# Kernel optimization log

Hardware: AMD Instinct MI355X
Metric: run time of the kernel (lower is better)

The kernel has to match this reference:

```python
import jax, jax.numpy as jnp
import numpy as np

QBITS = 8
QMIN, QMAX = -(2 ** (QBITS - 1)), 2 ** (QBITS - 1) - 1  # qint8: -128..127


def fq_act(x):
    """Per-tensor affine fake-quant (observer = min/max of tensor), with STE."""
    mn = jnp.minimum(jnp.min(x), 0.0)
    mx = jnp.maximum(jnp.max(x), 0.0)
    scale = jnp.maximum((mx - mn) / (QMAX - QMIN), 1e-8)
    zp = QMIN - jnp.round(mn / scale)
    q = jnp.clip(jnp.round(x / scale) + zp, QMIN, QMAX)
    y = (q - zp) * scale
    return x + jax.lax.stop_gradient(y - x)


def fq_w(w):
    """Per-tensor symmetric weight fake-quant, with STE."""
    scale = jnp.maximum(jnp.max(jnp.abs(w)) / QMAX, 1e-8)
    y = jnp.clip(jnp.round(w / scale), QMIN, QMAX) * scale
    return w + jax.lax.stop_gradient(y - w)


def setup_inputs() -> dict:
    key = jax.random.key(0)
    ks = jax.random.split(key, 8)
    B, T, F, K = 32, 1024, 512, 31
    return {
        "x": jax.random.normal(ks[0], (B, T, F), jnp.float32),
        "ln_scale": jnp.ones((F,), jnp.float32),
        "ln_bias": jnp.zeros((F,), jnp.float32),
        "w1": jax.random.normal(ks[1], (2 * F, F), jnp.float32) * 0.02,
        "b1": jax.random.normal(ks[2], (2 * F,), jnp.float32) * 0.02,
        "dw_w": jax.random.normal(ks[3], (F, 1, K), jnp.float32) * 0.1,
        "dw_b": jax.random.normal(ks[4], (F,), jnp.float32) * 0.02,
        "bn_gamma": jnp.ones((F,), jnp.float32),
        "bn_beta": jnp.zeros((F,), jnp.float32),
        "bn_mean": jnp.zeros((F,), jnp.float32),
        "bn_var": jax.random.uniform(ks[5], (F,), jnp.float32, 0.5, 1.5),
        "w2": jax.random.normal(ks[6], (F, F), jnp.float32) * 0.02,
        "b2": jax.random.normal(ks[7], (F,), jnp.float32) * 0.02,
    }


def reference(x, ln_scale, ln_bias, w1, b1, dw_w, dw_b,
              bn_gamma, bn_beta, bn_mean, bn_var, w2, b2):
    F = x.shape[-1]
    # --- custom L1 layer norm, fake-quant in/out ---
    t = fq_act(x)
    t = t - jnp.mean(t, axis=-1, keepdims=True)
    t = t / (jnp.sum(jnp.abs(t), axis=-1, keepdims=True) / F + 1e-5)
    t = t * ln_scale + ln_bias
    t = fq_act(t)
    # --- pointwise conv 1 (linear F -> 2F), quant-wrapped ---
    t = fq_act(t)
    t = jnp.einsum("btf,of->bto", t, fq_w(w1)) + b1
    t = fq_act(t)
    # --- GLU, quant-wrapped ---
    t = fq_act(t)
    a, g = jnp.split(t, 2, axis=-1)
    t = a * jax.nn.sigmoid(g)
    t = fq_act(t)
    # --- depthwise conv over time, quant-wrapped ---
    t = jnp.transpose(t, (0, 2, 1))  # [B,F,T]
    t = fq_act(t)
    t = jax.lax.conv_general_dilated(
        t, fq_w(dw_w), window_strides=(1,), padding=[((dw_w.shape[-1] - 1) // 2,) * 2],
        dimension_numbers=("NCH", "OIH", "NCH"), feature_group_count=F,
    ) + dw_b[:, None]
    t = fq_act(t)
    # --- batch norm (eval mode, running stats), quant-wrapped ---
    t = fq_act(t)
    t = (t - bn_mean[:, None]) * (bn_gamma[:, None] / jnp.sqrt(bn_var[:, None] + 1e-5)) + bn_beta[:, None]
    t = fq_act(t)
    t = jnp.transpose(t, (0, 2, 1))  # [B,T,F]
    # --- SiLU activation, quant-wrapped ---
    t = fq_act(t)
    t = jax.nn.silu(t)
    t = fq_act(t)
    # --- pointwise conv 2 (linear F -> F), quant-wrapped ---
    t = fq_act(t)
    t = jnp.einsum("btf,of->bto", t, fq_w(w2)) + b2
    t = fq_act(t)
    return t  # dropout is identity at eval
```

## Files before the change

### kernel.cpp

```cpp
#include <hip/hip_runtime.h>
#include <stdint.h>
#include <math.h>

#define INF __builtin_inff()

typedef __attribute__((ext_vector_type(4))) float f32x4;
typedef __attribute__((ext_vector_type(8))) short s16x8;
typedef __attribute__((ext_vector_type(4))) short s16x4;
typedef __attribute__((ext_vector_type(4))) char c8x4;

#define S_XMN 0
#define S_XMX 1
#define S_T1MN 2
#define S_T1MX 3
#define S_T4MN 4
#define S_T4MX 5
#define S_T7MN 6
#define S_T7MX 7
#define S_CVMN 8
#define S_CVMX 9
#define S_BNMN 10
#define S_BNMX 11
#define S_SIMN 12
#define S_SIMX 13
#define S_T18MN 14
#define S_T18MX 15
#define S_W1 16
#define S_W2 17
#define S_DW 18
#define NSLOT 19

#define NTOT 16777216L

__device__ __forceinline__ unsigned enc(float f) {
  unsigned u = __float_as_uint(f);
  return (u & 0x80000000u) ? ~u : (u | 0x80000000u);
}
__device__ __forceinline__ float dec(unsigned k) {
  return (k & 0x80000000u) ? __uint_as_float(k & 0x7FFFFFFFu) : __uint_as_float(~k);
}

struct FQ { float s, zp; };

__device__ __forceinline__ FQ fq_params(float mn_t, float mx_t) {
  float mn = fminf(mn_t, 0.0f), mx = fmaxf(mx_t, 0.0f);
  FQ p;
  p.s = fmaxf((mx - mn) / 255.0f, 1e-8f);
  p.zp = -128.0f - rintf(mn / p.s);
  return p;
}
__device__ __forceinline__ float fq_apply(float x, FQ p) {
  float q = rintf(x / p.s) + p.zp;
  q = fminf(fmaxf(q, -128.0f), 127.0f);
  return (q - p.zp) * p.s;
}
__device__ __forceinline__ float fq_qmz(float x, FQ p) {
  float q = rintf(x / p.s) + p.zp;
  q = fminf(fmaxf(q, -128.0f), 127.0f);
  return q - p.zp;
}
__device__ __forceinline__ int qidx(float x, FQ p) {
  float q = rintf(x / p.s) + p.zp;
  q = fminf(fmaxf(q, -128.0f), 127.0f);
  return (int)q + 128;
}
__device__ __forceinline__ void fq_pair(const unsigned* slots, int idx, FQ& p1, FQ& p2) {
  float mn = dec(slots[idx]), mx = dec(slots[idx + 1]);
  p1 = fq_params(mn, mx);
  float ymn = fq_apply(mn, p1), ymx = fq_apply(mx, p1);
  p2 = fq_params(ymn, ymx);
}
__device__ __forceinline__ unsigned short to_bf16(float v) {
  return (unsigned short)(__float_as_uint(v) >> 16);
}

__device__ __forceinline__ void mm_block_atomic(float mn, float mx, unsigned* smn, unsigned* smx) {
#pragma unroll
  for (int o = 32; o > 0; o >>= 1) {
    mn = fminf(mn, __shfl_down(mn, o, 64));
    mx = fmaxf(mx, __shfl_down(mx, o, 64));
  }
  __shared__ float rmn[16], rmx[16];
  int lane = threadIdx.x & 63, wid = threadIdx.x >> 6;
  int nw = blockDim.x >> 6;
  __syncthreads();
  if (lane == 0) { rmn[wid] = mn; rmx[wid] = mx; }
  __syncthreads();
  if (threadIdx.x == 0) {
    for (int i = 1; i < nw; ++i) { mn = fminf(mn, rmn[i]); mx = fmaxf(mx, rmx[i]); }
    atomicMin(smn, enc(mn));
    atomicMax(smx, enc(mx));
  }
}

__device__ __forceinline__ float wave_sum(float v) {
#pragma unroll
  for (int o = 1; o < 64; o <<= 1) v += __shfl_xor(v, o, 64);
  return v;
}

__global__ void k_init(unsigned* __restrict__ slots, const float* __restrict__ gm,
                       const float* __restrict__ vr, float* __restrict__ gs) {
  int i = threadIdx.x;
  if (i < NSLOT) slots[i] = (i < 16) ? ((i & 1) ? enc(-INF) : enc(INF)) : enc(0.0f);
  gs[i] = gm[i] / sqrtf(vr[i] + 1e-5f);
}

__global__ __launch_bounds__(256) void k_redmm(const float* __restrict__ x, unsigned* __restrict__ slots) {
  long i = ((long)blockIdx.x * 256 + threadIdx.x) * 4;
  const long stride = (long)2048 * 256 * 4;
  float mn = INF, mx = -INF;
  for (; i < NTOT; i += stride) {
    f32x4 v = *(const f32x4*)(x + i);
    mn = fminf(mn, fminf(fminf(v.x, v.y), fminf(v.z, v.w)));
    mx = fmaxf(mx, fmaxf(fmaxf(v.x, v.y), fmaxf(v.z, v.w)));
  }
  mm_block_atomic(mn, mx, slots + S_XMN, slots + S_XMX);
}

__global__ __launch_bounds__(256) void k_wabs(const float* __restrict__ w1, const float* __restrict__ w2,
                                              const float* __restrict__ dw, unsigned* __restrict__ slots) {
  int b = blockIdx.x;
  const float* p; int slot; long base;
  if (b < 2048) { p = w1; slot = S_W1; base = (long)b * 256; }
  else if (b < 3072) { p = w2; slot = S_W2; base = (long)(b - 2048) * 256; }
  else { p = dw; slot = S_DW; base = (long)(b - 3072) * 256; }
  float v = fabsf(p[base + threadIdx.x]);
#pragma unroll
  for (int o = 32; o > 0; o >>= 1) v = fmaxf(v, __shfl_down(v, o, 64));
  __shared__ float r[4];
  int lane = threadIdx.x & 63, wid = threadIdx.x >> 6;
  if (lane == 0) r[wid] = v;
  __syncthreads();
  if (threadIdx.x == 0) {
    v = fmaxf(fmaxf(r[0], r[1]), fmaxf(r[2], r[3]));
    atomicMax(slots + slot, enc(v));
  }
}

__global__ __launch_bounds__(256) void k_wq(const float* __restrict__ w1, const float* __restrict__ w2,
    const float* __restrict__ dw, unsigned short* __restrict__ w1q, unsigned short* __restrict__ w2q,
    float* __restrict__ dwq, const unsigned* __restrict__ slots) {
  int b = blockIdx.x;
  if (b < 2048) {
    float s = fmaxf(dec(slots[S_W1]) / 127.0f, 1e-8f);
    long i = (long)b * 256 + threadIdx.x;
    float q = fminf(fmaxf(rintf(w1[i] / s), -128.0f), 127.0f);
    w1q[i] = to_bf16(q);
  } else if (b < 3072) {
    float s = fmaxf(dec(slots[S_W2]) / 127.0f, 1e-8f);
    long i = (long)(b - 2048) * 256 + threadIdx.x;
    float q = fminf(fmaxf(rintf(w2[i] / s), -128.0f), 127.0f);
    w2q[i] = to_bf16(q);
  } else {
    float s = fmaxf(dec(slots[S_DW]) / 127.0f, 1e-8f);
    long i = (long)(b - 3072) * 256 + threadIdx.x;
    float q = fminf(fmaxf(rintf(dw[i] / s), -128.0f), 127.0f);
    dwq[i] = q;
  }
}

__device__ __forceinline__ void ln_row_wave(const float* __restrict__ xr, int lane, FQ p0,
    const f32x4& sc0, const f32x4& sc1, const f32x4& bi0, const f32x4& bi1,
    f32x4& o0, f32x4& o1) {
  f32x4 v0 = *(const f32x4*)(xr + lane * 4);
  f32x4 v1 = *(const f32x4*)(xr + 256 + lane * 4);
  float a[8];
#pragma unroll
  for (int j = 0; j < 4; ++j) { a[j] = fq_apply(v0[j], p0); a[4 + j] = fq_apply(v1[j], p0); }
  float s = a[0] + a[1] + a[2] + a[3] + a[4] + a[5] + a[6] + a[7];
  float mean = wave_sum(s) / 512.0f;
#pragma unroll
  for (int j = 0; j < 8; ++j) a[j] -= mean;
  float l1 = fabsf(a[0]) + fabsf(a[1]) + fabsf(a[2]) + fabsf(a[3])
           + fabsf(a[4]) + fabsf(a[5]) + fabsf(a[6]) + fabsf(a[7]);
  float denom = wave_sum(l1) / 512.0f + 1e-5f;
#pragma unroll
  for (int j = 0; j < 4; ++j) {
    o0[j] = (a[j] / denom) * sc0[j] + bi0[j];
    o1[j] = (a[4 + j] / denom) * sc1[j] + bi1[j];
  }
}

__global__ __launch_bounds__(256) void k_lnmm(const float* __restrict__ x, const float* __restrict__ lns,
    const float* __restrict__ lnb, unsigned* __restrict__ slots) {
  FQ p0 = fq_params(dec(slots[S_XMN]), dec(slots[S_XMX]));
  int lane = threadIdx.x & 63, wv = threadIdx.x >> 6;
  long gw = (long)blockIdx.x * 4 + wv;
  f32x4 sc0 = *(const f32x4*)(lns + lane * 4);
  f32x4 sc1 = *(const f32x4*)(lns + 256 + lane * 4);
  f32x4 bi0 = *(const f32x4*)(lnb + lane * 4);
  f32x4 bi1 = *(const f32x4*)(lnb + 256 + lane * 4);
  float lmn = INF, lmx = -INF;
  for (int r = 0; r < 4; ++r) {
    long row = gw + (long)r * 8192;
    f32x4 o0, o1;
    ln_row_wave(x + row * 512, lane, p0, sc0, sc1, bi0, bi1, o0, o1);
#pragma unroll
    for (int j = 0; j < 4; ++j) {
      lmn = fminf(lmn, fminf(o0[j], o1[j]));
      lmx = fmaxf(lmx, fmaxf(o0[j], o1[j]));
    }
  }
  mm_block_atomic(lmn, lmx, slots + S_T1MN, slots + S_T1MX);
}

__global__ __launch_bounds__(256) void k_qa(const float* __restrict__ x, const float* __restrict__ lns,
    const float* __restrict__ lnb, unsigned short* __restrict__ A1, const unsigned* __restrict__ slots) {
  __shared__ unsigned short lut[256];
  FQ p0 = fq_params(dec(slots[S_XMN]), dec(slots[S_XMX]));
  FQ p1, p2; fq_pair(slots, S_T1MN, p1, p2);
  {
    int i = threadIdx.x;
    float y1 = ((float)(i - 128) - p1.zp) * p1.s;
    lut[i] = to_bf16(fq_qmz(y1, p2));
  }
  __syncthreads();
  int lane = threadIdx.x & 63, wv = threadIdx.x >> 6;
  long gw = (long)blockIdx.x * 4 + wv;
  f32x4 sc0 = *(const f32x4*)(lns + lane * 4);
  f32x4 sc1 = *(const f32x4*)(lns + 256 + lane * 4);
  f32x4 bi0 = *(const f32x4*)(lnb + lane * 4);
  f32x4 bi1 = *(const f32x4*)(lnb + 256 + lane * 4);
  for (int r = 0; r < 4; ++r) {
    long row = gw + (long)r * 8192;
    f32x4 o0, o1;
    ln_row_wave(x + row * 512, lane, p0, sc0, sc1, bi0, bi1, o0, o1);
    s16x4 q0, q1;
#pragma unroll
    for (int j = 0; j < 4; ++j) {
      q0[j] = (short)lut[qidx(o0[j], p1)];
      q1[j] = (short)lut[qidx(o1[j], p1)];
    }
    *(s16x4*)(A1 + row * 512 + lane * 4) = q0;
    *(s16x4*)(A1 + row * 512 + 256 + lane * 4) = q1;
  }
}

__global__ __launch_bounds__(256) void k_gemm(const unsigned short* __restrict__ A,
    const unsigned short* __restrict__ Bm, const float* __restrict__ bias,
    float* __restrict__ C, int N, unsigned* __restrict__ slots, int mmIdx, int wIdx, int omIdx) {
  __shared__ __align__(16) unsigned short lA[128 * 64];
  __shared__ __align__(16) unsigned short lB[128 * 64];
  FQ p1, p2; fq_pair(slots, mmIdx, p1, p2);
  float sw = fmaxf(dec(slots[wIdx]) / 127.0f, 1e-8f);
  float sAB = p2.s * sw;
  int tid = threadIdx.x;
  int m0 = blockIdx.y * 128, n0 = blockIdx.x * 128;
  int lane = tid & 63, wid = tid >> 6;
  int wm = (wid >> 1) * 64, wn = (wid & 1) * 64;
  const f32x4 fz = {0.0f, 0.0f, 0.0f, 0.0f};
  f32x4 acc[4][4];
#pragma unroll
  for (int mi = 0; mi < 4; ++mi)
#pragma unroll
    for (int ni = 0; ni < 4; ++ni) acc[mi][ni] = fz;
  int sr = tid >> 1;
  int scu = (tid & 1) * 32;
  int swz = (sr & 7) * 8;
  const unsigned short* Ag = A + (long)(m0 + sr) * 512 + scu;
  const unsigned short* Bg = Bm + (long)(n0 + sr) * 512 + scu;
  int fr = lane & 15;
  int fc = (lane >> 4) * 8;
  for (int kt = 0; kt < 8; ++kt) {
    s16x8 ra[4], rb[4];
#pragma unroll
    for (int j = 0; j < 4; ++j) {
      ra[j] = *(const s16x8*)(Ag + kt * 64 + j * 8);
      rb[j] = *(const s16x8*)(Bg + kt * 64 + j * 8);
    }
    __syncthreads();
#pragma unroll
    for (int j = 0; j < 4; ++j) {
      *(s16x8*)&lA[sr * 64 + ((scu + j * 8) ^ swz)] = ra[j];
      *(s16x8*)&lB[sr * 64 + ((scu + j * 8) ^ swz)] = rb[j];
    }
    __syncthreads();
#pragma unroll
    for (int ks = 0; ks < 2; ++ks) {
      s16x8 af[4], bfv[4];
#pragma unroll
      for (int mi = 0; mi < 4; ++mi) {
        int r = wm + mi * 16 + fr;
        af[mi] = *(const s16x8*)&lA[r * 64 + ((ks * 32 + fc) ^ ((r & 7) * 8))];
      }
#pragma unroll
      for (int ni = 0; ni < 4; ++ni) {
        int r = wn + ni * 16 + fr;
        bfv[ni] = *(const s16x8*)&lB[r * 64 + ((ks * 32 + fc) ^ ((r & 7) * 8))];
      }
#pragma unroll
      for (int mi = 0; mi < 4; ++mi)
#pragma unroll
        for (int ni = 0; ni < 4; ++ni)
          acc[mi][ni] = __builtin_amdgcn_mfma_f32_16x16x32_bf16(af[mi], bfv[ni], acc[mi][ni], 0, 0, 0);
    }
  }
  float lmn = INF, lmx = -INF;
  int rb0 = m0 + wm + ((lane >> 4) << 2);
  int cb0 = n0 + wn + (lane & 15);
#pragma unroll
  for (int mi = 0; mi < 4; ++mi) {
#pragma unroll
    for (int ni = 0; ni < 4; ++ni) {
      int col = cb0 + ni * 16;
      float bv = bias[col];
#pragma unroll
      for (int r = 0; r < 4; ++r) {
        int rowi = rb0 + mi * 16 + r;
        float v = sAB * acc[mi][ni][r] + bv;
        C[(long)rowi * N + col] = v;
        lmn = fminf(lmn, v); lmx = fmaxf(lmx, v);
      }
    }
  }
  mm_block_atomic(lmn, lmx, slots + omIdx, slots + omIdx + 1);
}

__global__ __launch_bounds__(256) void k_glu(const float* __restrict__ t4, float* __restrict__ t7,
                                             unsigned* __restrict__ slots) {
  __shared__ float lut[256];
  FQ p1, p2; fq_pair(slots, S_T4MN, p1, p2);
  {
    int i = threadIdx.x;
    float y1 = ((float)(i - 128) - p1.zp) * p1.s;
    lut[i] = fq_apply(y1, p2);
  }
  __syncthreads();
  long i = ((long)blockIdx.x * 256 + threadIdx.x) * 4;
  const long stride = (long)2048 * 256 * 4;
  float lmn = INF, lmx = -INF;
  for (; i < NTOT; i += stride) {
    long r = i >> 9;
    int c = (int)(i & 511);
    const float* pa = t4 + r * 1024 + c;
    f32x4 av = *(const f32x4*)pa;
    f32x4 gv = *(const f32x4*)(pa + 512);
    f32x4 o;
#pragma unroll
    for (int j = 0; j < 4; ++j) {
      float a = lut[qidx(av[j], p1)];
      float g = lut[qidx(gv[j], p1)];
      float y = a * (1.0f / (1.0f + expf(-g)));
      o[j] = y;
      lmn = fminf(lmn, y); lmx = fmaxf(lmx, y);
    }
    *(f32x4*)(t7 + i) = o;
  }
  mm_block_atomic(lmn, lmx, slots + S_T7MN, slots + S_T7MX);
}

__global__ __launch_bounds__(256) void k_qt7(const float* __restrict__ t7, signed char* __restrict__ q7,
                                             const unsigned* __restrict__ slots) {
  __shared__ signed char lutq[256];
  FQ p1, p2; fq_pair(slots, S_T7MN, p1, p2);
  {
    int i = threadIdx.x;
    float y1 = ((float)(i - 128) - p1.zp) * p1.s;
    float q = fminf(fmaxf(rintf(y1 / p2.s) + p2.zp, -128.0f), 127.0f);
    lutq[i] = (signed char)(int)q;
  }
  __syncthreads();
  long i = ((long)blockIdx.x * 256 + threadIdx.x) * 4;
  const long stride = (long)2048 * 256 * 4;
  for (; i < NTOT; i += stride) {
    f32x4 v = *(const f32x4*)(t7 + i);
    c8x4 o;
#pragma unroll
    for (int j = 0; j < 4; ++j) o[j] = lutq[qidx(v[j], p1)];
    *(c8x4*)(q7 + i) = o;
  }
}

__global__ __launch_bounds__(256) void k_conv(const signed char* __restrict__ q7,
    const float* __restrict__ dwq, const float* __restrict__ dwb,
    float* __restrict__ out, unsigned* __restrict__ slots) {
  FQ p1, p2; fq_pair(slots, S_T7MN, p1, p2);
  float sdw = fmaxf(dec(slots[S_DW]) / 127.0f, 1e-8f);
  float scv = p2.s * sdw;
  float zp2 = p2.zp;
  int t0 = blockIdx.x * 32;
  int f = blockIdx.y * 256 + threadIdx.x;
  int b = blockIdx.z;
  const signed char* base = q7 + (long)b * 1024 * 512 + f;
  float col[62];
#pragma unroll
  for (int r = 0; r < 62; ++r) {
    int t = t0 - 15 + r;
    float q = 0.0f;
    if ((unsigned)t < 1024u) q = (float)(int)base[(long)t * 512] - zp2;
    col[r] = q;
  }
  float w31[31];
#pragma unroll
  for (int k = 0; k < 31; ++k) w31[k] = dwq[f * 31 + k];
  float bias = dwb[f];
  float* orow = out + ((long)b * 1024 + t0) * 512 + f;
  float lmn = INF, lmx = -INF;
#pragma unroll
  for (int j = 0; j < 32; ++j) {
    float acc = 0.0f;
#pragma unroll
    for (int k = 0; k < 31; ++k) acc += col[j + k] * w31[k];
    float v = scv * acc + bias;
    lmn = fminf(lmn, v); lmx = fmaxf(lmx, v);
    orow[(long)j * 512] = v;
  }
  mm_block_atomic(lmn, lmx, slots + S_CVMN, slots + S_CVMX);
}

__global__ __launch_bounds__(256) void k_qcv_bnmm(const float* __restrict__ conv,
    signed char* __restrict__ qcv, const float* __restrict__ gs, const float* __restrict__ mu,
    const float* __restrict__ bt, unsigned* __restrict__ slots) {
  __shared__ signed char lutq[256];
  FQ p1, p2; fq_pair(slots, S_CVMN, p1, p2);
  {
    int i = threadIdx.x;
    float y1 = ((float)(i - 128) - p1.zp) * p1.s;
    float q = fminf(fmaxf(rintf(y1 / p2.s) + p2.zp, -128.0f), 127.0f);
    lutq[i] = (signed char)(int)q;
  }
  __syncthreads();
  float s2 = p2.s, zp2 = p2.zp;
  long i = ((long)blockIdx.x * 256 + threadIdx.x) * 4;
  const long stride = (long)2048 * 256 * 4;
  float lmn = INF, lmx = -INF;
  for (; i < NTOT; i += stride) {
    int f0 = (int)(i & 511);
    f32x4 v = *(const f32x4*)(conv + i);
    f32x4 g4 = *(const f32x4*)(gs + f0);
    f32x4 m4 = *(const f32x4*)(mu + f0);
    f32x4 b4 = *(const f32x4*)(bt + f0);
    c8x4 o;
#pragma unroll
    for (int j = 0; j < 4; ++j) {
      signed char qc = lutq[qidx(v[j], p1)];
      o[j] = qc;
      float y2 = ((float)(int)qc - zp2) * s2;
      float z = (y2 - m4[j]) * g4[j] + b4[j];
      lmn = fminf(lmn, z); lmx = fmaxf(lmx, z);
    }
    *(c8x4*)(qcv + i) = o;
  }
  mm_block_atomic(lmn, lmx, slots + S_BNMN, slots + S_BNMX);
}

__global__ __launch_bounds__(256) void k_silumm(const signed char* __restrict__ qcv,
    const float* __restrict__ gs, const float* __restrict__ mu, const float* __restrict__ bt,
    unsigned* __restrict__ slots) {
  __shared__ float lutb[256];
  FQ c1, c2; fq_pair(slots, S_CVMN, c1, c2);
  FQ b1q, b2q; fq_pair(slots, S_BNMN, b1q, b2q);
  {
    int i = threadIdx.x;
    float y1 = ((float)(i - 128) - b1q.zp) * b1q.s;
    lutb[i] = fq_apply(y1, b2q);
  }
  __syncthreads();
  float s2 = c2.s, zp2 = c2.zp;
  long i = ((long)blockIdx.x * 256 + threadIdx.x) * 4;
  const long stride = (long)2048 * 256 * 4;
  float lmn = INF, lmx = -INF;
  for (; i < NTOT; i += stride) {
    int f0 = (int)(i & 511);
    c8x4 qv = *(const c8x4*)(qcv + i);
    f32x4 g4 = *(const f32x4*)(gs + f0);
    f32x4 m4 = *(const f32x4*)(mu + f0);
    f32x4 b4 = *(const f32x4*)(bt + f0);
#pragma unroll
    for (int j = 0; j < 4; ++j) {
      float y2 = ((float)(int)qv[j] - zp2) * s2;
      float z = (y2 - m4[j]) * g4[j] + b4[j];
      float z2 = lutb[qidx(z, b1q)];
      float si = z2 * (1.0f / (1.0f + expf(-z2)));
      lmn = fminf(lmn, si); lmx = fmaxf(lmx, si);
    }
  }
  mm_block_atomic(lmn, lmx, slots + S_SIMN, slots + S_SIMX);
}

__global__ __launch_bounds__(256) void k_q2(const signed char* __restrict__ qcv,
    const float* __restrict__ gs, const float* __restrict__ mu, const float* __restrict__ bt,
    unsigned short* __restrict__ A2, const unsigned* __restrict__ slots) {
  __shared__ float lutb[256];
  __shared__ unsigned short luts[256];
  FQ c1, c2; fq_pair(slots, S_CVMN, c1, c2);
  FQ b1q, b2q; fq_pair(slots, S_BNMN, b1q, b2q);
  FQ s1q, s2q; fq_pair(slots, S_SIMN, s1q, s2q);
  {
    int i = threadIdx.x;
    float yb = ((float)(i - 128) - b1q.zp) * b1q.s;
    lutb[i] = fq_apply(yb, b2q);
    float ys = ((float)(i - 128) - s1q.zp) * s1q.s;
    luts[i] = to_bf16(fq_qmz(ys, s2q));
  }
  __syncthreads();
  float s2 = c2.s, zp2 = c2.zp;
  long i = ((long)blockIdx.x * 256 + threadIdx.x) * 4;
  const long stride = (long)2048 * 256 * 4;
  for (; i < NTOT; i += stride) {
    int f0 = (int)(i & 511);
    c8x4 qv = *(const c8x4*)(qcv + i);
    f32x4 g4 = *(const f32x4*)(gs + f0);
    f32x4 m4 = *(const f32x4*)(mu + f0);
    f32x4 b4 = *(const f32x4*)(bt + f0);
    s16x4 o;
#pragma unroll
    for (int j = 0; j < 4; ++j) {
      float y2 = ((float)(int)qv[j] - zp2) * s2;
      float z = (y2 - m4[j]) * g4[j] + b4[j];
      float z2 = lutb[qidx(z, b1q)];
      float si = z2 * (1.0f / (1.0f + expf(-z2)));
      o[j] = (short)luts[qidx(si, s1q)];
    }
    *(s16x4*)(A2 + i) = o;
  }
}

__global__ __launch_bounds__(256) void k_final(const float* __restrict__ t18, float* __restrict__ out,
                                               const unsigned* __restrict__ slots) {
  FQ p = fq_params(dec(slots[S_T18MN]), dec(slots[S_T18MX]));
  long i = ((long)blockIdx.x * 256 + threadIdx.x) * 4;
  const long stride = (long)2048 * 256 * 4;
  for (; i < NTOT; i += stride) {
    f32x4 v = *(const f32x4*)(t18 + i);
    f32x4 o;
#pragma unroll
    for (int j = 0; j < 4; ++j) o[j] = fq_apply(v[j], p);
    *(f32x4*)(out + i) = o;
  }
}

extern "C" void kernel_launch(void* const* d_in, const int* in_sizes, int n_in,
                              void* d_out, int out_size, void* d_ws, size_t ws_size,
                              hipStream_t stream) {
  const float* x   = (const float*)d_in[0];
  const float* lns = (const float*)d_in[1];
  const float* lnb = (const float*)d_in[2];
  const float* w1  = (const float*)d_in[3];
  const float* b1  = (const float*)d_in[4];
  const float* dw  = (const float*)d_in[5];
  const float* dwb = (const float*)d_in[6];
  const float* gm  = (const float*)d_in[7];
  const float* bt  = (const float*)d_in[8];
  const float* mu  = (const float*)d_in[9];
  const float* vr  = (const float*)d_in[10];
  const float* w2  = (const float*)d_in[11];
  const float* b2  = (const float*)d_in[12];
  float* out = (float*)d_out;
  char* ws = (char*)d_ws;

  const size_t OFF_B = 134217728;
  const size_t OFF_D = OFF_B + 67108864;
  const size_t OFF_W = OFF_D + 33554432;
  const size_t NEED = OFF_W + 1048576 + 524288 + 63488 + 2048 + 256;
  if (ws_size < NEED) return;

  float* buf0 = (float*)ws;
  float* bufB = (float*)(ws + OFF_B);
  unsigned short* bufD = (unsigned short*)(ws + OFF_D);
  signed char* q7  = (signed char*)(ws + OFF_D);
  signed char* qcv = (signed char*)(ws + OFF_D + 16777216);
  unsigned short* A2 = (unsigned short*)ws;
  unsigned short* w1q = (unsigned short*)(ws + OFF_W);
  unsigned short* w2q = (unsigned short*)(ws + OFF_W + 1048576);
  float* dwq = (float*)(ws + OFF_W + 1048576 + 524288);
  float* gs  = (float*)(ws + OFF_W + 1048576 + 524288 + 63488);
  unsigned* slots = (unsigned*)(ws + OFF_W + 1048576 + 524288 + 63488 + 2048);

  k_init<<<1, 512, 0, stream>>>(slots, gm, vr, gs);
  k_wabs<<<3134, 256, 0, stream>>>(w1, w2, dw, slots);
  k_wq<<<3134, 256, 0, stream>>>(w1, w2, dw, w1q, w2q, dwq, slots);
  k_redmm<<<2048, 256, 0, stream>>>(x, slots);
  k_lnmm<<<2048, 256, 0, stream>>>(x, lns, lnb, slots);
  k_qa<<<2048, 256, 0, stream>>>(x, lns, lnb, bufD, slots);
  k_gemm<<<dim3(8, 256), 256, 0, stream>>>(bufD, w1q, b1, buf0, 1024, slots, S_T1MN, S_W1, S_T4MN);
  k_glu<<<2048, 256, 0, stream>>>(buf0, bufB, slots);
  k_qt7<<<2048, 256, 0, stream>>>(bufB, q7, slots);
  k_conv<<<dim3(32, 2, 32), 256, 0, stream>>>(q7, dwq, dwb, buf0, slots);
  k_qcv_bnmm<<<2048, 256, 0, stream>>>(buf0, qcv, gs, mu, bt, slots);
  k_silumm<<<2048, 256, 0, stream>>>(qcv, gs, mu, bt, slots);
  k_q2<<<2048, 256, 0, stream>>>(qcv, gs, mu, bt, A2, slots);
  k_gemm<<<dim3(4, 256), 256, 0, stream>>>(A2, w2q, b2, bufB, 512, slots, S_SIMN, S_W2, S_T18MN);
  k_final<<<2048, 256, 0, stream>>>(bufB, out, slots);
}
```

Baseline: 748.7 us.

## Shrink intermediate traffic with int8/pair codes, recompute conv, fold LUTs

The layer-norm min/max pass now writes int8 quantized input codes, and the second LN pass reads those codes instead of reloading fp32 x. GLU stores packed 8-bit code pairs instead of fp32 output, and the downstream quant kernel rebuilds values from small lookup tables. The depthwise conv now runs twice, once for min/max only and once writing int8 codes fused with batch-norm stats, which drops the fp32 conv buffer. Sigmoid and SiLU are precomputed into per-code LUTs, and GEMM block indices are remapped across XCDs. The trade is recomputing the conv and doing extra LUT setup in exchange for much less HBM traffic.

```diff
diff --git a/kernel.cpp b/kernel.cpp
--- a/kernel.cpp
+++ b/kernel.cpp
@@ -64,6 +64,11 @@
   q = fminf(fmaxf(q, -128.0f), 127.0f);
   return (int)q + 128;
 }
+__device__ __forceinline__ int qcode(float x, FQ p) {
+  float q = rintf(x / p.s) + p.zp;
+  q = fminf(fmaxf(q, -128.0f), 127.0f);
+  return (int)q;
+}
 __device__ __forceinline__ void fq_pair(const unsigned* slots, int idx, FQ& p1, FQ& p2) {
   float mn = dec(slots[idx]), mx = dec(slots[idx + 1]);
   p1 = fq_params(mn, mx);
@@ -160,14 +165,8 @@
   }
 }
 
-__device__ __forceinline__ void ln_row_wave(const float* __restrict__ xr, int lane, FQ p0,
-    const f32x4& sc0, const f32x4& sc1, const f32x4& bi0, const f32x4& bi1,
-    f32x4& o0, f32x4& o1) {
-  f32x4 v0 = *(const f32x4*)(xr + lane * 4);
-  f32x4 v1 = *(const f32x4*)(xr + 256 + lane * 4);
-  float a[8];
-#pragma unroll
-  for (int j = 0; j < 4; ++j) { a[j] = fq_apply(v0[j], p0); a[4 + j] = fq_apply(v1[j], p0); }
+__device__ __forceinline__ void ln_core(float* a, const f32x4& sc0, const f32x4& sc1,
+                                        const f32x4& bi0, const f32x4& bi1) {
   float s = a[0] + a[1] + a[2] + a[3] + a[4] + a[5] + a[6] + a[7];
   float mean = wave_sum(s) / 512.0f;
 #pragma unroll
@@ -177,13 +176,13 @@
   float denom = wave_sum(l1) / 512.0f + 1e-5f;
 #pragma unroll
   for (int j = 0; j < 4; ++j) {
-    o0[j] = (a[j] / denom) * sc0[j] + bi0[j];
-    o1[j] = (a[4 + j] / denom) * sc1[j] + bi1[j];
+    a[j]     = fmaf(a[j] / denom,     sc0[j], bi0[j]);
+    a[4 + j] = fmaf(a[4 + j] / denom, sc1[j], bi1[j]);
   }
 }
 
 __global__ __launch_bounds__(256) void k_lnmm(const float* __restrict__ x, const float* __restrict__ lns,
-    const float* __restrict__ lnb, unsigned* __restrict__ slots) {
+    const float* __restrict__ lnb, signed char* __restrict__ qx, unsigned* __restrict__ slots) {
   FQ p0 = fq_params(dec(slots[S_XMN]), dec(slots[S_XMX]));
   int lane = threadIdx.x & 63, wv = threadIdx.x >> 6;
   long gw = (long)blockIdx.x * 4 + wv;
@@ -194,18 +193,27 @@
   float lmn = INF, lmx = -INF;
   for (int r = 0; r < 4; ++r) {
     long row = gw + (long)r * 8192;
-    f32x4 o0, o1;
-    ln_row_wave(x + row * 512, lane, p0, sc0, sc1, bi0, bi1, o0, o1);
-#pragma unroll
-    for (int j = 0; j < 4; ++j) {
-      lmn = fminf(lmn, fminf(o0[j], o1[j]));
-      lmx = fmaxf(lmx, fmaxf(o0[j], o1[j]));
-    }
+    f32x4 v0 = *(const f32x4*)(x + row * 512 + lane * 4);
+    f32x4 v1 = *(const f32x4*)(x + row * 512 + 256 + lane * 4);
+    float a[8];
+    c8x4 c0, c1;
+#pragma unroll
+    for (int j = 0; j < 4; ++j) {
+      int q0 = qcode(v0[j], p0), q1 = qcode(v1[j], p0);
+      c0[j] = (signed char)q0; c1[j] = (signed char)q1;
+      a[j]     = ((float)q0 - p0.zp) * p0.s;
+      a[4 + j] = ((float)q1 - p0.zp) * p0.s;
+    }
+    *(c8x4*)(qx + row * 512 + lane * 4) = c0;
+    *(c8x4*)(qx + row * 512 + 256 + lane * 4) = c1;
+    ln_core(a, sc0, sc1, bi0, bi1);
+#pragma unroll
+    for (int j = 0; j < 8; ++j) { lmn = fminf(lmn, a[j]); lmx = fmaxf(lmx, a[j]); }
   }
   mm_block_atomic(lmn, lmx, slots + S_T1MN, slots + S_T1MX);
 }
 
-__global__ __launch_bounds__(256) void k_qa(const float* __restrict__ x, const float* __restrict__ lns,
+__global__ __launch_bounds__(256) void k_qa(const signed char* __restrict__ qx, const float* __restrict__ lns,
     const float* __restrict__ lnb, unsigned short* __restrict__ A1, const unsigned* __restrict__ slots) {
   __shared__ unsigned short lut[256];
   FQ p0 = fq_params(dec(slots[S_XMN]), dec(slots[S_XMX]));
@@ -224,13 +232,20 @@
   f32x4 bi1 = *(const f32x4*)(lnb + 256 + lane * 4);
   for (int r = 0; r < 4; ++r) {
     long row = gw + (long)r * 8192;
-    f32x4 o0, o1;
-    ln_row_wave(x + row * 512, lane, p0, sc0, sc1, bi0, bi1, o0, o1);
+    c8x4 c0 = *(const c8x4*)(qx + row * 512 + lane * 4);
+    c8x4 c1 = *(const c8x4*)(qx + row * 512 + 256 + lane * 4);
+    float a[8];
+#pragma unroll
+    for (int j = 0; j < 4; ++j) {
+      a[j]     = ((float)(int)c0[j] - p0.zp) * p0.s;
+      a[4 + j] = ((float)(int)c1[j] - p0.zp) * p0.s;
+    }
+    ln_core(a, sc0, sc1, bi0, bi1);
     s16x4 q0, q1;
 #pragma unroll
     for (int j = 0; j < 4; ++j) {
-      q0[j] = (short)lut[qidx(o0[j], p1)];
-      q1[j] = (short)lut[qidx(o1[j], p1)];
+      q0[j] = (short)lut[qidx(a[j], p1)];
+      q1[j] = (short)lut[qidx(a[4 + j], p1)];
     }
     *(s16x4*)(A1 + row * 512 + lane * 4) = q0;
     *(s16x4*)(A1 + row * 512 + 256 + lane * 4) = q1;
@@ -246,7 +261,12 @@
   float sw = fmaxf(dec(slots[wIdx]) / 127.0f, 1e-8f);
   float sAB = p2.s * sw;
   int tid = threadIdx.x;
-  int m0 = blockIdx.y * 128, n0 = blockIdx.x * 128;
+  int nbx = gridDim.x;
+  int total = nbx * gridDim.y;
+  int id = blockIdx.y * nbx + blockIdx.x;
+  int chunk = total >> 3;
+  int d = (id & 7) * chunk + (id >> 3);
+  int m0 = (d / nbx) * 128, n0 = (d % nbx) * 128;
   int lane = tid & 63, wid = tid >> 6;
   int wm = (wid >> 1) * 64, wn = (wid & 1) * 64;
   const f32x4 fz = {0.0f, 0.0f, 0.0f, 0.0f};
@@ -317,14 +337,16 @@
   mm_block_atomic(lmn, lmx, slots + omIdx, slots + omIdx + 1);
 }
 
-__global__ __launch_bounds__(256) void k_glu(const float* __restrict__ t4, float* __restrict__ t7,
+__global__ __launch_bounds__(256) void k_glu(const float* __restrict__ t4, unsigned short* __restrict__ pair,
                                              unsigned* __restrict__ slots) {
-  __shared__ float lut[256];
+  __shared__ float lutf[256];
+  __shared__ float sglut[256];
   FQ p1, p2; fq_pair(slots, S_T4MN, p1, p2);
   {
     int i = threadIdx.x;
-    float y1 = ((float)(i - 128) - p1.zp) * p1.s;
-    lut[i] = fq_apply(y1, p2);
+    float y2 = fq_apply(((float)(i - 128) - p1.zp) * p1.s, p2);
+    lutf[i] = y2;
+    sglut[i] = 1.0f / (1.0f + expf(-y2));
   }
   __syncthreads();
   long i = ((long)blockIdx.x * 256 + threadIdx.x) * 4;
@@ -336,26 +358,33 @@
     const float* pa = t4 + r * 1024 + c;
     f32x4 av = *(const f32x4*)pa;
     f32x4 gv = *(const f32x4*)(pa + 512);
-    f32x4 o;
-#pragma unroll
-    for (int j = 0; j < 4; ++j) {
-      float a = lut[qidx(av[j], p1)];
-      float g = lut[qidx(gv[j], p1)];
-      float y = a * (1.0f / (1.0f + expf(-g)));
-      o[j] = y;
+    s16x4 o;
+#pragma unroll
+    for (int j = 0; j < 4; ++j) {
+      int qa = qidx(av[j], p1);
+      int qg = qidx(gv[j], p1);
+      o[j] = (short)(unsigned short)(qa | (qg << 8));
+      float y = lutf[qa] * sglut[qg];
       lmn = fminf(lmn, y); lmx = fmaxf(lmx, y);
     }
-    *(f32x4*)(t7 + i) = o;
+    *(s16x4*)(pair + i) = o;
   }
   mm_block_atomic(lmn, lmx, slots + S_T7MN, slots + S_T7MX);
 }
 
-__global__ __launch_bounds__(256) void k_qt7(const float* __restrict__ t7, signed char* __restrict__ q7,
+__global__ __launch_bounds__(256) void k_qt7(const unsigned short* __restrict__ pair,
+                                             signed char* __restrict__ q7,
                                              const unsigned* __restrict__ slots) {
+  __shared__ float lutf[256];
+  __shared__ float sglut[256];
   __shared__ signed char lutq[256];
+  FQ g1, g2; fq_pair(slots, S_T4MN, g1, g2);
   FQ p1, p2; fq_pair(slots, S_T7MN, p1, p2);
   {
     int i = threadIdx.x;
+    float y2 = fq_apply(((float)(i - 128) - g1.zp) * g1.s, g2);
+    lutf[i] = y2;
+    sglut[i] = 1.0f / (1.0f + expf(-y2));
     float y1 = ((float)(i - 128) - p1.zp) * p1.s;
     float q = fminf(fmaxf(rintf(y1 / p2.s) + p2.zp, -128.0f), 127.0f);
     lutq[i] = (signed char)(int)q;
@@ -364,21 +393,37 @@
   long i = ((long)blockIdx.x * 256 + threadIdx.x) * 4;
   const long stride = (long)2048 * 256 * 4;
   for (; i < NTOT; i += stride) {
-    f32x4 v = *(const f32x4*)(t7 + i);
+    s16x4 pv = *(const s16x4*)(pair + i);
     c8x4 o;
 #pragma unroll
-    for (int j = 0; j < 4; ++j) o[j] = lutq[qidx(v[j], p1)];
+    for (int j = 0; j < 4; ++j) {
+      unsigned u = (unsigned short)pv[j];
+      float y = lutf[u & 255] * sglut[u >> 8];
+      o[j] = lutq[qidx(y, p1)];
+    }
     *(c8x4*)(q7 + i) = o;
   }
 }
 
+template<int STORE>
 __global__ __launch_bounds__(256) void k_conv(const signed char* __restrict__ q7,
     const float* __restrict__ dwq, const float* __restrict__ dwb,
-    float* __restrict__ out, unsigned* __restrict__ slots) {
+    signed char* __restrict__ qcv, const float* __restrict__ gs, const float* __restrict__ mu,
+    const float* __restrict__ bt, unsigned* __restrict__ slots) {
+  __shared__ signed char lutq[256];
   FQ p1, p2; fq_pair(slots, S_T7MN, p1, p2);
   float sdw = fmaxf(dec(slots[S_DW]) / 127.0f, 1e-8f);
   float scv = p2.s * sdw;
   float zp2 = p2.zp;
+  FQ c1, c2;
+  if (STORE) {
+    fq_pair(slots, S_CVMN, c1, c2);
+    int i = threadIdx.x;
+    float y1 = ((float)(i - 128) - c1.zp) * c1.s;
+    float q = fminf(fmaxf(rintf(y1 / c2.s) + c2.zp, -128.0f), 127.0f);
+    lutq[i] = (signed char)(int)q;
+    __syncthreads();
+  }
   int t0 = blockIdx.x * 32;
   int f = blockIdx.y * 256 + threadIdx.x;
   int b = blockIdx.z;
@@ -395,66 +440,40 @@
 #pragma unroll
   for (int k = 0; k < 31; ++k) w31[k] = dwq[f * 31 + k];
   float bias = dwb[f];
-  float* orow = out + ((long)b * 1024 + t0) * 512 + f;
+  float gsv = 0.f, muv = 0.f, btv = 0.f;
+  if (STORE) { gsv = gs[f]; muv = mu[f]; btv = bt[f]; }
+  signed char* orow = STORE ? (qcv + ((long)b * 1024 + t0) * 512 + f) : nullptr;
   float lmn = INF, lmx = -INF;
 #pragma unroll
   for (int j = 0; j < 32; ++j) {
     float acc = 0.0f;
 #pragma unroll
     for (int k = 0; k < 31; ++k) acc += col[j + k] * w31[k];
-    float v = scv * acc + bias;
-    lmn = fminf(lmn, v); lmx = fmaxf(lmx, v);
-    orow[(long)j * 512] = v;
-  }
-  mm_block_atomic(lmn, lmx, slots + S_CVMN, slots + S_CVMX);
-}
-
-__global__ __launch_bounds__(256) void k_qcv_bnmm(const float* __restrict__ conv,
-    signed char* __restrict__ qcv, const float* __restrict__ gs, const float* __restrict__ mu,
-    const float* __restrict__ bt, unsigned* __restrict__ slots) {
-  __shared__ signed char lutq[256];
-  FQ p1, p2; fq_pair(slots, S_CVMN, p1, p2);
-  {
-    int i = threadIdx.x;
-    float y1 = ((float)(i - 128) - p1.zp) * p1.s;
-    float q = fminf(fmaxf(rintf(y1 / p2.s) + p2.zp, -128.0f), 127.0f);
-    lutq[i] = (signed char)(int)q;
-  }
-  __syncthreads();
-  float s2 = p2.s, zp2 = p2.zp;
-  long i = ((long)blockIdx.x * 256 + threadIdx.x) * 4;
-  const long stride = (long)2048 * 256 * 4;
-  float lmn = INF, lmx = -INF;
-  for (; i < NTOT; i += stride) {
-    int f0 = (int)(i & 511);
-    f32x4 v = *(const f32x4*)(conv + i);
-    f32x4 g4 = *(const f32x4*)(gs + f0);
-    f32x4 m4 = *(const f32x4*)(mu + f0);
-    f32x4 b4 = *(const f32x4*)(bt + f0);
-    c8x4 o;
-#pragma unroll
-    for (int j = 0; j < 4; ++j) {
-      signed char qc = lutq[qidx(v[j], p1)];
-      o[j] = qc;
-      float y2 = ((float)(int)qc - zp2) * s2;
-      float z = (y2 - m4[j]) * g4[j] + b4[j];
+    float v = fmaf(scv, acc, bias);
+    if (STORE) {
+      signed char qc = lutq[qidx(v, c1)];
+      orow[(long)j * 512] = qc;
+      float y2 = ((float)(int)qc - c2.zp) * c2.s;
+      float z = fmaf(y2 - muv, gsv, btv);
       lmn = fminf(lmn, z); lmx = fmaxf(lmx, z);
-    }
-    *(c8x4*)(qcv + i) = o;
-  }
-  mm_block_atomic(lmn, lmx, slots + S_BNMN, slots + S_BNMX);
+    } else {
+      lmn = fminf(lmn, v); lmx = fmaxf(lmx, v);
+    }
+  }
+  if (STORE) mm_block_atomic(lmn, lmx, slots + S_BNMN, slots + S_BNMX);
+  else       mm_block_atomic(lmn, lmx, slots + S_CVMN, slots + S_CVMX);
 }
 
 __global__ __launch_bounds__(256) void k_silumm(const signed char* __restrict__ qcv,
     const float* __restrict__ gs, const float* __restrict__ mu, const float* __restrict__ bt,
     unsigned* __restrict__ slots) {
-  __shared__ float lutb[256];
+  __shared__ float sillut[256];
   FQ c1, c2; fq_pair(slots, S_CVMN, c1, c2);
   FQ b1q, b2q; fq_pair(slots, S_BNMN, b1q, b2q);
   {
     int i = threadIdx.x;
-    float y1 = ((float)(i - 128) - b1q.zp) * b1q.s;
-    lutb[i] = fq_apply(y1, b2q);
+    float z2 = fq_apply(((float)(i - 128) - b1q.zp) * b1q.s, b2q);
+    sillut[i] = z2 * (1.0f / (1.0f + expf(-z2)));
   }
   __syncthreads();
   float s2 = c2.s, zp2 = c2.zp;
@@ -470,9 +489,8 @@
 #pragma unroll
     for (int j = 0; j < 4; ++j) {
       float y2 = ((float)(int)qv[j] - zp2) * s2;
-      float z = (y2 - m4[j]) * g4[j] + b4[j];
-      float z2 = lutb[qidx(z, b1q)];
-      float si = z2 * (1.0f / (1.0f + expf(-z2)));
+      float z = fmaf(y2 - m4[j], g4[j], b4[j]);
+      float si = sillut[qidx(z, b1q)];
       lmn = fminf(lmn, si); lmx = fmaxf(lmx, si);
     }
   }
@@ -482,17 +500,16 @@
 __global__ __launch_bounds__(256) void k_q2(const signed char* __restrict__ qcv,
     const float* __restrict__ gs, const float* __restrict__ mu, const float* __restrict__ bt,
     unsigned short* __restrict__ A2, const unsigned* __restrict__ slots) {
-  __shared__ float lutb[256];
-  __shared__ unsigned short luts[256];
+  __shared__ unsigned short lutc[256];
   FQ c1, c2; fq_pair(slots, S_CVMN, c1, c2);
   FQ b1q, b2q; fq_pair(slots, S_BNMN, b1q, b2q);
   FQ s1q, s2q; fq_pair(slots, S_SIMN, s1q, s2q);
   {
     int i = threadIdx.x;
-    float yb = ((float)(i - 128) - b1q.zp) * b1q.s;
-    lutb[i] = fq_apply(yb, b2q);
-    float ys = ((float)(i - 128) - s1q.zp) * s1q.s;
-    luts[i] = to_bf16(fq_qmz(ys, s2q));
+    float z2 = fq_apply(((float)(i - 128) - b1q.zp) * b1q.s, b2q);
+    float si = z2 * (1.0f / (1.0f + expf(-z2)));
+    float ys = ((float)(qidx(si, s1q) - 128) - s1q.zp) * s1q.s;
+    lutc[i] = to_bf16(fq_qmz(ys, s2q));
   }
   __syncthreads();
   float s2 = c2.s, zp2 = c2.zp;
@@ -508,10 +525,8 @@
 #pragma unroll
     for (int j = 0; j < 4; ++j) {
       float y2 = ((float)(int)qv[j] - zp2) * s2;
-      float z = (y2 - m4[j]) * g4[j] + b4[j];
-      float z2 = lutb[qidx(z, b1q)];
-      float si = z2 * (1.0f / (1.0f + expf(-z2)));
-      o[j] = (short)luts[qidx(si, s1q)];
+      float z = fmaf(y2 - m4[j], g4[j], b4[j]);
+      o[j] = (short)lutc[qidx(z, b1q)];
     }
     *(s16x4*)(A2 + i) = o;
   }
@@ -550,37 +565,41 @@
   float* out = (float*)d_out;
   char* ws = (char*)d_ws;
 
-  const size_t OFF_B = 134217728;
-  const size_t OFF_D = OFF_B + 67108864;
-  const size_t OFF_W = OFF_D + 33554432;
-  const size_t NEED = OFF_W + 1048576 + 524288 + 63488 + 2048 + 256;
+  const size_t O_A2  = 16777216;
+  const size_t O_T18 = 50331648;
+  const size_t O_A1  = 134217728;
+  const size_t O_QX  = 167772160;
+  const size_t O_WQ  = 184549376;
+  const size_t NEED = O_WQ + 1048576 + 524288 + 63488 + 2048 + 256;
   if (ws_size < NEED) return;
 
-  float* buf0 = (float*)ws;
-  float* bufB = (float*)(ws + OFF_B);
-  unsigned short* bufD = (unsigned short*)(ws + OFF_D);
-  signed char* q7  = (signed char*)(ws + OFF_D);
-  signed char* qcv = (signed char*)(ws + OFF_D + 16777216);
-  unsigned short* A2 = (unsigned short*)ws;
-  unsigned short* w1q = (unsigned short*)(ws + OFF_W);
-  unsigned short* w2q = (unsigned short*)(ws + OFF_W + 1048576);
-  float* dwq = (float*)(ws + OFF_W + 1048576 + 524288);
-  float* gs  = (float*)(ws + OFF_W + 1048576 + 524288 + 63488);
-  unsigned* slots = (unsigned*)(ws + OFF_W + 1048576 + 524288 + 63488 + 2048);
+  float* t4   = (float*)ws;
+  signed char* qcv = (signed char*)ws;
+  unsigned short* A2 = (unsigned short*)(ws + O_A2);
+  float* t18  = (float*)(ws + O_T18);
+  unsigned short* A1 = (unsigned short*)(ws + O_A1);
+  unsigned short* pair = (unsigned short*)(ws + O_A1);
+  signed char* qx = (signed char*)(ws + O_QX);
+  signed char* q7 = (signed char*)(ws + O_QX);
+  unsigned short* w1q = (unsigned short*)(ws + O_WQ);
+  unsigned short* w2q = (unsigned short*)(ws + O_WQ + 1048576);
+  float* dwq = (float*)(ws + O_WQ + 1048576 + 524288);
+  float* gs  = (float*)(ws + O_WQ + 1048576 + 524288 + 63488);
+  unsigned* slots = (unsigned*)(ws + O_WQ + 1048576 + 524288 + 63488 + 2048);
 
   k_init<<<1, 512, 0, stream>>>(slots, gm, vr, gs);
   k_wabs<<<3134, 256, 0, stream>>>(w1, w2, dw, slots);
   k_wq<<<3134, 256, 0, stream>>>(w1, w2, dw, w1q, w2q, dwq, slots);
   k_redmm<<<2048, 256, 0, stream>>>(x, slots);
-  k_lnmm<<<2048, 256, 0, stream>>>(x, lns, lnb, slots);
-  k_qa<<<2048, 256, 0, stream>>>(x, lns, lnb, bufD, slots);
-  k_gemm<<<dim3(8, 256), 256, 0, stream>>>(bufD, w1q, b1, buf0, 1024, slots, S_T1MN, S_W1, S_T4MN);
-  k_glu<<<2048, 256, 0, stream>>>(buf0, bufB, slots);
-  k_qt7<<<2048, 256, 0, stream>>>(bufB, q7, slots);
-  k_conv<<<dim3(32, 2, 32), 256, 0, stream>>>(q7, dwq, dwb, buf0, slots);
-  k_qcv_bnmm<<<2048, 256, 0, stream>>>(buf0, qcv, gs, mu, bt, slots);
+  k_lnmm<<<2048, 256, 0, stream>>>(x, lns, lnb, qx, slots);
+  k_qa<<<2048, 256, 0, stream>>>(qx, lns, lnb, A1, slots);
+  k_gemm<<<dim3(8, 256), 256, 0, stream>>>(A1, w1q, b1, t4, 1024, slots, S_T1MN, S_W1, S_T4MN);
+  k_glu<<<2048, 256, 0, stream>>>(t4, pair, slots);
+  k_qt7<<<2048, 256, 0, stream>>>(pair, q7, slots);
+  k_conv<0><<<dim3(32, 2, 32), 256, 0, stream>>>(q7, dwq, dwb, nullptr, gs, mu, bt, slots);
+  k_conv<1><<<dim3(32, 2, 32), 256, 0, stream>>>(q7, dwq, dwb, qcv, gs, mu, bt, slots);
   k_silumm<<<2048, 256, 0, stream>>>(qcv, gs, mu, bt, slots);
   k_q2<<<2048, 256, 0, stream>>>(qcv, gs, mu, bt, A2, slots);
-  k_gemm<<<dim3(4, 256), 256, 0, stream>>>(A2, w2q, b2, bufB, 512, slots, S_SIMN, S_W2, S_T18MN);
-  k_final<<<2048, 256, 0, stream>>>(bufB, out, slots);
-}
+  k_gemm<<<dim3(4, 256), 256, 0, stream>>>(A2, w2q, b2, t18, 512, slots, S_SIMN, S_W2, S_T18MN);
+  k_final<<<2048, 256, 0, stream>>>(t18, out, slots);
+}
```

Result: faster. 731.6 us (-2.3%).
